# Kernel optimization log

Measured on AMD Instinct MI355X. Metric: run time of the kernel, lower is better.

Reference implementation:

```python
import jax, jax.numpy as jnp
import numpy as np

N_NODES = 50000
N_EDGES = 1_600_000
D_IN, D_HID, D_OUT = 128, 512, 64


def _graph_conv(h, src, dst, W_rel, b_rel, W_root, n_nodes):
    # PyG GraphConv with aggr='add':
    #   out_i = W_rel @ (sum_{j->i} h_j) + b_rel + W_root @ h_i
    agg = jax.ops.segment_sum(h[src], dst, num_segments=n_nodes)  # [N, d]
    return agg @ W_rel + b_rel + h @ W_root


def setup_inputs() -> dict:
    key = jax.random.key(0)
    ks = jax.random.split(key, 12)
    def glorot(k, shape):
        fan_in, fan_out = shape
        lim = (6.0 / (fan_in + fan_out)) ** 0.5
        return jax.random.uniform(k, shape, jnp.float32, -lim, lim)
    x = jax.random.normal(ks[0], (N_NODES, D_IN), jnp.float32)
    edge_index = jax.random.randint(ks[1], (2, N_EDGES), 0, N_NODES, jnp.int64)
    return {
        "x": x,
        "W1_rel": glorot(ks[2], (D_IN, D_HID)),
        "b1": jnp.zeros((D_HID,), jnp.float32),
        "W1_root": glorot(ks[3], (D_IN, D_HID)),
        "W2_rel": glorot(ks[4], (D_HID, D_HID)),
        "b2": jnp.zeros((D_HID,), jnp.float32),
        "W2_root": glorot(ks[5], (D_HID, D_HID)),
        "W3_rel": glorot(ks[6], (D_HID, D_HID)),
        "b3": jnp.zeros((D_HID,), jnp.float32),
        "W3_root": glorot(ks[7], (D_HID, D_HID)),
        "W_lin": glorot(ks[8], (D_HID, D_OUT)),
        "b_lin": jnp.zeros((D_OUT,), jnp.float32),
        "edge_index": edge_index,
    }


def reference(x, W1_rel, b1, W1_root, W2_rel, b2, W2_root,
              W3_rel, b3, W3_root, W_lin, b_lin, edge_index):
    n = x.shape[0]
    src, dst = edge_index[0], edge_index[1]
    h = jax.nn.relu(_graph_conv(x, src, dst, W1_rel, b1, W1_root, n))
    h = jax.nn.relu(_graph_conv(h, src, dst, W2_rel, b2, W2_root, n))
    h = jax.nn.relu(_graph_conv(h, src, dst, W3_rel, b3, W3_root, n))
    node_embed = h
    # dropout is identity in eval mode; final linear head
    logits = h @ W_lin + b_lin
    return (logits, node_embed)
```

## Files before the change

kernel.cpp:

```cpp
#include <hip/hip_runtime.h>


typedef unsigned short u16;
typedef unsigned int u32;
typedef unsigned char u8;

#define NN 50000
#define NE 1600000
#define MPAD 50176
#define GRID_M ((NN + 127) / 128)
#define NBKT 98
#define CAP 20480
#define STG 18432

using frag8 = __attribute__((ext_vector_type(8))) short;
using f32x4 = __attribute__((ext_vector_type(4))) float;
using f32x2 = __attribute__((ext_vector_type(2))) float;

__device__ __forceinline__ u16 f2bf(float f) {
  u32 u = __float_as_uint(f);
  u32 r = u + 0x7fffu + ((u >> 16) & 1u);
  return (u16)(r >> 16);
}
__device__ __forceinline__ float lo2f(u32 u) { return __uint_as_float(u << 16); }
__device__ __forceinline__ float hi2f(u32 u) { return __uint_as_float(u & 0xffff0000u); }
__device__ __forceinline__ u32 pack2(float a, float b) {
  return (u32)f2bf(a) | ((u32)f2bf(b) << 16);
}

__device__ __forceinline__ void g2l16(const void* g, void* l) {
  __builtin_amdgcn_global_load_lds((const __attribute__((address_space(1))) void*)g,
                                   (__attribute__((address_space(3))) void*)l, 16, 0, 0);
}


__global__ void zero_i32(int* p, int n) {
  int i = blockIdx.x * 256 + threadIdx.x;
  if (i < n) p[i] = 0;
}

__global__ __launch_bounds__(256) void p1bin(const int* __restrict__ src,
                                             const int* __restrict__ dst,
                                             int* __restrict__ gcur,
                                             u32* __restrict__ region, int ne) {
  __shared__ u32 lbuf[NBKT * 64];
  __shared__ int lcnt[NBKT];
  __shared__ int gbase[NBKT];
  const int tid = threadIdx.x;
  if (tid < NBKT) lcnt[tid] = 0;
  __syncthreads();
  const int base = blockIdx.x * 2048;
#pragma unroll
  for (int j = 0; j < 8; ++j) {
    int i = base + j * 256 + tid;
    if (i < ne) {
      int d = dst[i];
      int s = src[i];
      int b = d >> 9;
      u32 entry = ((u32)(d & 511) << 16) | (u32)s;
      int slot = atomicAdd(&lcnt[b], 1);
      if (slot < 64) lbuf[b * 64 + slot] = entry;
      else {
        int g = atomicAdd(&gcur[b], 1);
        region[(size_t)b * CAP + g] = entry;
      }
    }
  }
  __syncthreads();
  if (tid < NBKT) {
    int c = min(lcnt[tid], 64);
    gbase[tid] = atomicAdd(&gcur[tid], c);
  }
  __syncthreads();
  const int wv = tid >> 6, lane = tid & 63;
  for (int b = wv; b < NBKT; b += 4) {
    int c = min(lcnt[b], 64);
    int gb = gbase[b];
    for (int s2 = lane; s2 < c; s2 += 64)
      region[(size_t)b * CAP + gb + s2] = lbuf[b * 64 + s2];
  }
}

__global__ void scan98(const int* __restrict__ gcur, int* __restrict__ bbase,
                       int* __restrict__ rs) {
  if (threadIdx.x == 0) {
    int run = 0;
    for (int b = 0; b < NBKT; ++b) {
      bbase[b] = run;
      run += gcur[b];
    }
    bbase[NBKT] = run;
    rs[NN] = run;
  }
}

__global__ __launch_bounds__(256) void p2build(const u32* __restrict__ region,
                                               const int* __restrict__ gcnt,
                                               const int* __restrict__ bbase,
                                               int* __restrict__ rs,
                                               u16* __restrict__ csr) {
  __shared__ int cnt[512];
  __shared__ int off[512];
  __shared__ int sh[256];
  __shared__ u16 stg[STG];
  const int b = blockIdx.x, tid = threadIdx.x;
  const int n0 = b * 512;
  const int nnb = min(512, NN - n0);
  const int ec = gcnt[b];
  const int gb = bbase[b];
  const u32* __restrict__ reg = region + (size_t)b * CAP;
  cnt[tid] = 0;
  cnt[tid + 256] = 0;
  __syncthreads();
  for (int i = tid; i < ec; i += 256) atomicAdd(&cnt[reg[i] >> 16], 1);
  __syncthreads();
  int c0 = cnt[2 * tid], c1 = cnt[2 * tid + 1];
  int s = c0 + c1;
  sh[tid] = s;
  __syncthreads();
  for (int o = 1; o < 256; o <<= 1) {
    int t2 = (tid >= o) ? sh[tid - o] : 0;
    __syncthreads();
    sh[tid] += t2;
    __syncthreads();
  }
  int base0 = sh[tid] - s;
  off[2 * tid] = base0;
  off[2 * tid + 1] = base0 + c0;
  __syncthreads();
  if (2 * tid < nnb) rs[n0 + 2 * tid] = gb + off[2 * tid];
  if (2 * tid + 1 < nnb) rs[n0 + 2 * tid + 1] = gb + off[2 * tid + 1];
  cnt[2 * tid] = off[2 * tid];
  cnt[2 * tid + 1] = off[2 * tid + 1];
  __syncthreads();
  for (int i = tid; i < ec; i += 256) {
    u32 e = reg[i];
    int slot = atomicAdd(&cnt[e >> 16], 1);
    u16 sv = (u16)(e & 0xffff);
    if (slot < STG) stg[slot] = sv;
    else csr[gb + slot] = sv;
  }
  __syncthreads();
  for (int i = tid; i < ec && i < STG; i += 256) csr[gb + i] = stg[i];
}


__global__ void f2bf_x(const float4* __restrict__ in, u16* __restrict__ out, int n4) {
  int i = blockIdx.x * 256 + threadIdx.x;
  if (i < n4) {
    float4 v = in[i];
    int node = i >> 5;
    int w = i & 31;
    uint2 o;
    o.x = pack2(v.x, v.y);
    o.y = pack2(v.z, v.w);
    *(uint2*)(out + (size_t)node * 256 + 128 + w * 4) = o;
  }
}

__global__ void wtrans(const float* __restrict__ Wa, int Ka, const float* __restrict__ Wb,
                       int Kb, int N, u16* __restrict__ out) {
  int idx = blockIdx.x * 256 + threadIdx.x;
  int Kt = Ka + Kb;
  if (idx >= N * Kt) return;
  int n = idx / Kt;
  int k = idx - n * Kt;
  float v = (k < Ka) ? Wa[(size_t)k * N + n] : Wb[(size_t)(k - Ka) * N + n];
  out[idx] = f2bf(v);
}


__global__ __launch_bounds__(256) void agg_bf128(const u16* __restrict__ H, int ldh,
                                                 u16* __restrict__ Out, int ldo,
                                                 const int* __restrict__ rs,
                                                 const u16* __restrict__ csr, int n) {
  int w = (blockIdx.x * 256 + threadIdx.x) >> 6;
  int lane = threadIdx.x & 63;
  if (w >= n) return;
  int beg = rs[w], end = rs[w + 1];
  float a0 = 0.f, a1 = 0.f;
  const size_t lo = (size_t)lane * 2;
  int e = beg;
  for (; e + 4 <= end; e += 4) {
    int s0 = csr[e], s1 = csr[e + 1], s2 = csr[e + 2], s3 = csr[e + 3];
    u32 v0 = *(const u32*)(H + (size_t)s0 * ldh + lo);
    u32 v1 = *(const u32*)(H + (size_t)s1 * ldh + lo);
    u32 v2 = *(const u32*)(H + (size_t)s2 * ldh + lo);
    u32 v3 = *(const u32*)(H + (size_t)s3 * ldh + lo);
    a0 += lo2f(v0); a1 += hi2f(v0);
    a0 += lo2f(v1); a1 += hi2f(v1);
    a0 += lo2f(v2); a1 += hi2f(v2);
    a0 += lo2f(v3); a1 += hi2f(v3);
  }
  for (; e < end; ++e) {
    u32 v = *(const u32*)(H + (size_t)csr[e] * ldh + lo);
    a0 += lo2f(v); a1 += hi2f(v);
  }
  *(u32*)(Out + (size_t)w * ldo + lo) = pack2(a0, a1);
}


__device__ __forceinline__ void accf8(float* a, uint2 v, float s) {
  f32x2 f01 = __builtin_amdgcn_cvt_pk_f32_fp8(v.x, false);
  f32x2 f23 = __builtin_amdgcn_cvt_pk_f32_fp8(v.x, true);
  f32x2 f45 = __builtin_amdgcn_cvt_pk_f32_fp8(v.y, false);
  f32x2 f67 = __builtin_amdgcn_cvt_pk_f32_fp8(v.y, true);
  a[0] = fmaf(f01.x, s, a[0]); a[1] = fmaf(f01.y, s, a[1]);
  a[2] = fmaf(f23.x, s, a[2]); a[3] = fmaf(f23.y, s, a[3]);
  a[4] = fmaf(f45.x, s, a[4]); a[5] = fmaf(f45.y, s, a[5]);
  a[6] = fmaf(f67.x, s, a[6]); a[7] = fmaf(f67.y, s, a[7]);
}

__global__ __launch_bounds__(256) void agg_fp8(const u8* __restrict__ H8,
                                               const float* __restrict__ sc,
                                               u16* __restrict__ Out,
                                               const int* __restrict__ rs,
                                               const u16* __restrict__ csr, int n) {
  int w = (blockIdx.x * 256 + threadIdx.x) >> 6;
  int lane = threadIdx.x & 63;
  if (w >= n) return;
  int beg = rs[w], end = rs[w + 1];
  float acc[8];
#pragma unroll
  for (int i = 0; i < 8; ++i) acc[i] = 0.f;
  const int half = lane >> 5;
  const size_t lo = (size_t)lane * 8;
  int e = beg;
  for (; e + 4 <= end; e += 4) {
    int s0 = csr[e], s1 = csr[e + 1], s2 = csr[e + 2], s3 = csr[e + 3];
    uint2 v0 = *(const uint2*)(H8 + (size_t)s0 * 512 + lo);
    uint2 v1 = *(const uint2*)(H8 + (size_t)s1 * 512 + lo);
    uint2 v2 = *(const uint2*)(H8 + (size_t)s2 * 512 + lo);
    uint2 v3 = *(const uint2*)(H8 + (size_t)s3 * 512 + lo);
    float c0 = sc[s0 * 2 + half];
    float c1 = sc[s1 * 2 + half];
    float c2 = sc[s2 * 2 + half];
    float c3 = sc[s3 * 2 + half];
    accf8(acc, v0, c0); accf8(acc, v1, c1);
    accf8(acc, v2, c2); accf8(acc, v3, c3);
  }
  for (; e < end; ++e) {
    int s0 = csr[e];
    uint2 v = *(const uint2*)(H8 + (size_t)s0 * 512 + lo);
    accf8(acc, v, sc[s0 * 2 + half]);
  }
  uint4 o;
  o.x = pack2(acc[0], acc[1]); o.y = pack2(acc[2], acc[3]);
  o.z = pack2(acc[4], acc[5]); o.w = pack2(acc[6], acc[7]);
  *(uint4*)(Out + (size_t)w * 512 + lo) = o;
}


__global__ __launch_bounds__(512, 4) void gemm256(
    const u16* __restrict__ A1, int lda1, const u16* __restrict__ A2, int lda2, int K1,
    int Ktot, const u16* __restrict__ Bt, const float* __restrict__ bias, int relu,
    u16* __restrict__ out_bf, int ldob, float* __restrict__ out_f32, int ldof,
    u8* __restrict__ out_fp8, float* __restrict__ out_sc, int M) {
  __shared__ u16 lA[128 * 32];
  __shared__ u16 lB[256 * 32];
  __shared__ u32 smaxu[128];
  const int tid = threadIdx.x;
  const int lane = tid & 63;
  const int wv = tid >> 6;
  const int wm = (wv >> 2) * 64;
  const int wn = (wv & 3) * 64;
  const int n0 = blockIdx.x * 256;
  const int m0 = blockIdx.y * 128;
  const int r15 = lane & 15;
  const int quad = lane >> 4;

  if (tid < 128) smaxu[tid] = 0;

  f32x4 acc[4][4];
#pragma unroll
  for (int i = 0; i < 4; ++i)
#pragma unroll
    for (int j = 0; j < 4; ++j) acc[i][j] = (f32x4){0.f, 0.f, 0.f, 0.f};

  for (int kk = 0; kk < Ktot; kk += 32) {
    const u16* Ab;
    int lda;
    if (kk < K1) { Ab = A1 + kk; lda = lda1; }
    else         { Ab = A2 + (kk - K1); lda = lda2; }
    {
      int row = tid >> 2;
      int kc = (tid & 3) * 8;
      g2l16(Ab + (size_t)(m0 + row) * lda + kc, &lA[tid * 8]);
    }
#pragma unroll
    for (int i = 0; i < 2; ++i) {
      int li = tid + i * 512;
      int nrow = li >> 2;
      int kc = (li & 3) * 8;
      g2l16(Bt + (size_t)(n0 + nrow) * Ktot + (kk + kc), &lB[li * 8]);
    }
    __syncthreads();
    frag8 af[4], bfr[4];
#pragma unroll
    for (int mt = 0; mt < 4; ++mt)
      af[mt] = *(const frag8*)&lA[(wm + mt * 16 + r15) * 32 + quad * 8];
#pragma unroll
    for (int nt = 0; nt < 4; ++nt)
      bfr[nt] = *(const frag8*)&lB[(wn + nt * 16 + r15) * 32 + quad * 8];
#pragma unroll
    for (int mt = 0; mt < 4; ++mt)
#pragma unroll
      for (int nt = 0; nt < 4; ++nt)
        acc[mt][nt] =
            __builtin_amdgcn_mfma_f32_16x16x32_bf16(af[mt], bfr[nt], acc[mt][nt], 0, 0, 0);
    __syncthreads();
  }

#pragma unroll
  for (int mt = 0; mt < 4; ++mt) {
#pragma unroll
    for (int r = 0; r < 4; ++r) {
      float rm = 0.f;
#pragma unroll
      for (int nt = 0; nt < 4; ++nt) {
        int c = n0 + wn + nt * 16 + r15;
        float v = acc[mt][nt][r] + bias[c];
        if (relu) v = fmaxf(v, 0.f);
        acc[mt][nt][r] = v;
        rm = fmaxf(rm, v);
      }
      if (out_fp8) {
        rm = fmaxf(rm, __shfl_xor(rm, 1));
        rm = fmaxf(rm, __shfl_xor(rm, 2));
        rm = fmaxf(rm, __shfl_xor(rm, 4));
        rm = fmaxf(rm, __shfl_xor(rm, 8));
        if (r15 == 0) atomicMax(&smaxu[wm + mt * 16 + quad * 4 + r], __float_as_uint(rm));
      }
    }
  }
  if (out_fp8) __syncthreads();

#pragma unroll
  for (int mt = 0; mt < 4; ++mt) {
    int rloc = wm + mt * 16 + quad * 4;
#pragma unroll
    for (int r = 0; r < 4; ++r) {
      int row = m0 + rloc + r;
      if (row < M) {
        float inv = 0.f;
        if (out_fp8) {
          float s = __uint_as_float(smaxu[rloc + r]);
          inv = (s > 0.f) ? 448.f / s : 0.f;
          if (r15 == 0 && wn == 0)
            out_sc[row * 2 + (n0 >> 8)] = (s > 0.f) ? s / 448.f : 0.f;
        }
#pragma unroll
        for (int nt = 0; nt < 4; ++nt) {
          int c = n0 + wn + nt * 16 + r15;
          float v = acc[mt][nt][r];
          if (out_f32) out_f32[(size_t)row * ldof + c] = v;
          if (out_bf) out_bf[(size_t)row * ldob + c] = f2bf(v);
        }
        if (out_fp8) {
          u32 u01 = (u32)__builtin_amdgcn_cvt_pk_fp8_f32(acc[mt][0][r] * inv,
                                                         acc[mt][1][r] * inv, 0, false);
          u32 u23 = (u32)__builtin_amdgcn_cvt_pk_fp8_f32(acc[mt][2][r] * inv,
                                                         acc[mt][3][r] * inv, 0, false);
          size_t rb = (size_t)row * 512 + n0 + wn + r15;
          out_fp8[rb] = (u8)(u01 & 0xff);
          out_fp8[rb + 16] = (u8)((u01 >> 8) & 0xff);
          out_fp8[rb + 32] = (u8)(u23 & 0xff);
          out_fp8[rb + 48] = (u8)((u23 >> 8) & 0xff);
        }
      }
    }
  }
}


__global__ __launch_bounds__(256) void gemm64(
    const u16* __restrict__ A1, int lda1, int Ktot, const u16* __restrict__ Bt,
    const float* __restrict__ bias, float* __restrict__ out_f32, int ldof, int M) {
  __shared__ u16 lA[128 * 32];
  __shared__ u16 lB[64 * 32];
  const int tid = threadIdx.x;
  const int lane = tid & 63;
  const int wv = tid >> 6;
  const int wm = (wv >> 1) * 64;
  const int wn = (wv & 1) * 32;
  const int m0 = blockIdx.x * 128;
  const int r15 = lane & 15;
  const int quad = lane >> 4;

  f32x4 acc[4][2];
#pragma unroll
  for (int i = 0; i < 4; ++i)
#pragma unroll
    for (int j = 0; j < 2; ++j) acc[i][j] = (f32x4){0.f, 0.f, 0.f, 0.f};

  for (int kk = 0; kk < Ktot; kk += 32) {
#pragma unroll
    for (int i = 0; i < 2; ++i) {
      int li = tid + i * 256;
      int row = li >> 2;
      int kc = (li & 3) * 8;
      g2l16(A1 + (size_t)(m0 + row) * lda1 + kk + kc, &lA[li * 8]);
    }
    {
      int nrow = tid >> 2;
      int kc = (tid & 3) * 8;
      if (tid < 256) g2l16(Bt + (size_t)nrow * Ktot + (kk + kc), &lB[tid * 8]);
    }
    __syncthreads();
    frag8 af[4], bfr[2];
#pragma unroll
    for (int mt = 0; mt < 4; ++mt)
      af[mt] = *(const frag8*)&lA[(wm + mt * 16 + r15) * 32 + quad * 8];
#pragma unroll
    for (int nt = 0; nt < 2; ++nt)
      bfr[nt] = *(const frag8*)&lB[(wn + nt * 16 + r15) * 32 + quad * 8];
#pragma unroll
    for (int mt = 0; mt < 4; ++mt)
#pragma unroll
      for (int nt = 0; nt < 2; ++nt)
        acc[mt][nt] =
            __builtin_amdgcn_mfma_f32_16x16x32_bf16(af[mt], bfr[nt], acc[mt][nt], 0, 0, 0);
    __syncthreads();
  }

#pragma unroll
  for (int mt = 0; mt < 4; ++mt) {
    int rbase = m0 + wm + mt * 16 + quad * 4;
#pragma unroll
    for (int r = 0; r < 4; ++r) {
      int row = rbase + r;
      if (row < M) {
#pragma unroll
        for (int nt = 0; nt < 2; ++nt) {
          int c = wn + nt * 16 + r15;
          out_f32[(size_t)row * ldof + c] = acc[mt][nt][r] + bias[c];
        }
      }
    }
  }
}


extern "C" void kernel_launch(void* const* d_in, const int* in_sizes, int n_in, void* d_out,
                              int out_size, void* d_ws, size_t ws_size, hipStream_t stream) {
  const float* x = (const float*)d_in[0];
  const float* W1r = (const float*)d_in[1];
  const float* b1 = (const float*)d_in[2];
  const float* W1o = (const float*)d_in[3];
  const float* W2r = (const float*)d_in[4];
  const float* b2 = (const float*)d_in[5];
  const float* W2o = (const float*)d_in[6];
  const float* W3r = (const float*)d_in[7];
  const float* b3 = (const float*)d_in[8];
  const float* W3o = (const float*)d_in[9];
  const float* Wl = (const float*)d_in[10];
  const float* bl = (const float*)d_in[11];
  const int* src = (const int*)d_in[12];
  const int* dst = src + NE;

  size_t off = 0;
  char* ws = (char*)d_ws;
  auto take = [&](size_t bytes) -> void* {
    void* p = ws + off;
    off = (off + bytes + 255) & ~(size_t)255;
    return p;
  };
  u16* h13 = (u16*)take((size_t)MPAD * 512 * 2);
  u16* h2 = (u16*)take((size_t)MPAD * 512 * 2);
  u16* aggB = (u16*)take((size_t)MPAD * 512 * 2);
  u16* aggx = aggB;
  u8* hfp8 = (u8*)take((size_t)MPAD * 512);
  float* scb = (float*)take((size_t)MPAD * 2 * 4);
  u16* wt1 = (u16*)take((size_t)512 * 256 * 2);
  u16* wt2 = (u16*)take((size_t)512 * 1024 * 2);
  u16* wt3 = (u16*)take((size_t)512 * 1024 * 2);
  u16* wtl = (u16*)take((size_t)64 * 512 * 2);
  u32* region = (u32*)take((size_t)NBKT * CAP * 4);
  int* gcur = (int*)take(128 * 4);
  int* bbase = (int*)take(128 * 4);
  int* rs = (int*)take((size_t)(NN + 1) * 4);
  u16* csr = (u16*)take((size_t)NE * 2);

  float* out_logits = (float*)d_out;
  float* out_embed = out_logits + (size_t)NN * 64;

  zero_i32<<<1, 128, 0, stream>>>(gcur, NBKT);
  p1bin<<<(NE + 2047) / 2048, 256, 0, stream>>>(src, dst, gcur, region, NE);
  scan98<<<1, 64, 0, stream>>>(gcur, bbase, rs);
  p2build<<<NBKT, 256, 0, stream>>>(region, gcur, bbase, rs, csr);

  f2bf_x<<<(NN * 32 + 255) / 256, 256, 0, stream>>>((const float4*)x, aggx, NN * 32);
  wtrans<<<(512 * 256 + 255) / 256, 256, 0, stream>>>(W1r, 128, W1o, 128, 512, wt1);
  wtrans<<<(512 * 1024 + 255) / 256, 256, 0, stream>>>(W2r, 512, W2o, 512, 512, wt2);
  wtrans<<<(512 * 1024 + 255) / 256, 256, 0, stream>>>(W3r, 512, W3o, 512, 512, wt3);
  wtrans<<<(64 * 512 + 255) / 256, 256, 0, stream>>>(Wl, 512, Wl, 0, 64, wtl);

  agg_bf128<<<(NN + 3) / 4, 256, 0, stream>>>(aggx + 128, 256, aggx, 256, rs, csr, NN);
  gemm256<<<dim3(2, GRID_M), 512, 0, stream>>>(aggx, 256, aggx, 256, 256, 256, wt1, b1, 1,
                                               h13, 512, (float*)nullptr, 0, hfp8, scb, NN);
  agg_fp8<<<(NN + 3) / 4, 256, 0, stream>>>(hfp8, scb, aggB, rs, csr, NN);
  gemm256<<<dim3(2, GRID_M), 512, 0, stream>>>(aggB, 512, h13, 512, 512, 1024, wt2, b2, 1,
                                               h2, 512, (float*)nullptr, 0, hfp8, scb, NN);
  agg_fp8<<<(NN + 3) / 4, 256, 0, stream>>>(hfp8, scb, aggB, rs, csr, NN);
  gemm256<<<dim3(2, GRID_M), 512, 0, stream>>>(aggB, 512, h2, 512, 512, 1024, wt3, b3, 1,
                                               h13, 512, out_embed, 512, (u8*)nullptr,
                                               (float*)nullptr, NN);
  gemm64<<<GRID_M, 256, 0, stream>>>(h13, 512, 512, wtl, bl, out_logits, 64, NN);
}
```

Measured before the change: 756.4 us.

## Widen aggregation gathers to 16-byte loads with edge-parallel lanes and shuffle reduction

```diff
diff --git a/kernel.cpp b/kernel.cpp
--- a/kernel.cpp
+++ b/kernel.cpp
@@ -170,6 +170,15 @@
 }
 
 
+__device__ __forceinline__ void accb(f32x2* a, uint4 v, float s) {
+  f32x2 sv = (f32x2){s, s};
+  f32x2 f;
+  f.x = lo2f(v.x); f.y = hi2f(v.x); a[0] += f * sv;
+  f.x = lo2f(v.y); f.y = hi2f(v.y); a[1] += f * sv;
+  f.x = lo2f(v.z); f.y = hi2f(v.z); a[2] += f * sv;
+  f.x = lo2f(v.w); f.y = hi2f(v.w); a[3] += f * sv;
+}
+
 __global__ __launch_bounds__(256) void agg_bf128(const u16* __restrict__ H, int ldh,
                                                  u16* __restrict__ Out, int ldo,
                                                  const int* __restrict__ rs,
@@ -178,37 +187,62 @@
   int lane = threadIdx.x & 63;
   if (w >= n) return;
   int beg = rs[w], end = rs[w + 1];
-  float a0 = 0.f, a1 = 0.f;
-  const size_t lo = (size_t)lane * 2;
+  const int q = lane >> 4;
+  const int lsub = lane & 15;
+  f32x2 acc[4];
+#pragma unroll
+  for (int i = 0; i < 4; ++i) acc[i] = (f32x2){0.f, 0.f};
+
   int e = beg;
-  for (; e + 4 <= end; e += 4) {
-    int s0 = csr[e], s1 = csr[e + 1], s2 = csr[e + 2], s3 = csr[e + 3];
-    u32 v0 = *(const u32*)(H + (size_t)s0 * ldh + lo);
-    u32 v1 = *(const u32*)(H + (size_t)s1 * ldh + lo);
-    u32 v2 = *(const u32*)(H + (size_t)s2 * ldh + lo);
-    u32 v3 = *(const u32*)(H + (size_t)s3 * ldh + lo);
-    a0 += lo2f(v0); a1 += hi2f(v0);
-    a0 += lo2f(v1); a1 += hi2f(v1);
-    a0 += lo2f(v2); a1 += hi2f(v2);
-    a0 += lo2f(v3); a1 += hi2f(v3);
-  }
-  for (; e < end; ++e) {
-    u32 v = *(const u32*)(H + (size_t)csr[e] * ldh + lo);
-    a0 += lo2f(v); a1 += hi2f(v);
-  }
-  *(u32*)(Out + (size_t)w * ldo + lo) = pack2(a0, a1);
-}
-
-
-__device__ __forceinline__ void accf8(float* a, uint2 v, float s) {
-  f32x2 f01 = __builtin_amdgcn_cvt_pk_f32_fp8(v.x, false);
-  f32x2 f23 = __builtin_amdgcn_cvt_pk_f32_fp8(v.x, true);
-  f32x2 f45 = __builtin_amdgcn_cvt_pk_f32_fp8(v.y, false);
-  f32x2 f67 = __builtin_amdgcn_cvt_pk_f32_fp8(v.y, true);
-  a[0] = fmaf(f01.x, s, a[0]); a[1] = fmaf(f01.y, s, a[1]);
-  a[2] = fmaf(f23.x, s, a[2]); a[3] = fmaf(f23.y, s, a[3]);
-  a[4] = fmaf(f45.x, s, a[4]); a[5] = fmaf(f45.y, s, a[5]);
-  a[6] = fmaf(f67.x, s, a[6]); a[7] = fmaf(f67.y, s, a[7]);
+  for (; e + 16 <= end; e += 16) {
+    int si[4];
+#pragma unroll
+    for (int u = 0; u < 4; ++u) si[u] = csr[e + 4 * u + q];
+    uint4 v[4];
+#pragma unroll
+    for (int u = 0; u < 4; ++u)
+      v[u] = *(const uint4*)(H + (size_t)si[u] * ldh + lsub * 8);
+#pragma unroll
+    for (int u = 0; u < 4; ++u) accb(acc, v[u], 1.f);
+  }
+  if (e < end) {
+#pragma unroll
+    for (int u = 0; u < 4; ++u) {
+      int ei = e + 4 * u + q;
+      int ec = min(ei, end - 1);
+      int s0 = csr[ec];
+      uint4 v = *(const uint4*)(H + (size_t)s0 * ldh + lsub * 8);
+      accb(acc, v, (ei < end) ? 1.f : 0.f);
+    }
+  }
+#pragma unroll
+  for (int i = 0; i < 4; ++i) {
+    acc[i].x += __shfl_xor(acc[i].x, 16);
+    acc[i].y += __shfl_xor(acc[i].y, 16);
+    acc[i].x += __shfl_xor(acc[i].x, 32);
+    acc[i].y += __shfl_xor(acc[i].y, 32);
+  }
+  if (lane < 32) {
+    int qq = lane >> 4;
+    uint2 o;
+    o.x = pack2(acc[qq * 2].x, acc[qq * 2].y);
+    o.y = pack2(acc[qq * 2 + 1].x, acc[qq * 2 + 1].y);
+    *(uint2*)(Out + (size_t)w * ldo + (lane & 15) * 8 + qq * 4) = o;
+  }
+}
+
+
+__device__ __forceinline__ void accp(f32x2* a, uint4 v, float s) {
+  f32x2 sv = (f32x2){s, s};
+  f32x2 f;
+  f = __builtin_amdgcn_cvt_pk_f32_fp8(v.x, false); a[0] += f * sv;
+  f = __builtin_amdgcn_cvt_pk_f32_fp8(v.x, true);  a[1] += f * sv;
+  f = __builtin_amdgcn_cvt_pk_f32_fp8(v.y, false); a[2] += f * sv;
+  f = __builtin_amdgcn_cvt_pk_f32_fp8(v.y, true);  a[3] += f * sv;
+  f = __builtin_amdgcn_cvt_pk_f32_fp8(v.z, false); a[4] += f * sv;
+  f = __builtin_amdgcn_cvt_pk_f32_fp8(v.z, true);  a[5] += f * sv;
+  f = __builtin_amdgcn_cvt_pk_f32_fp8(v.w, false); a[6] += f * sv;
+  f = __builtin_amdgcn_cvt_pk_f32_fp8(v.w, true);  a[7] += f * sv;
 }
 
 __global__ __launch_bounds__(256) void agg_fp8(const u8* __restrict__ H8,
@@ -220,34 +254,57 @@
   int lane = threadIdx.x & 63;
   if (w >= n) return;
   int beg = rs[w], end = rs[w + 1];
-  float acc[8];
-#pragma unroll
-  for (int i = 0; i < 8; ++i) acc[i] = 0.f;
-  const int half = lane >> 5;
-  const size_t lo = (size_t)lane * 8;
+  const int halfe = lane >> 5;
+  const int lsub = lane & 31;
+  const int shalf = lsub >> 4;
+  f32x2 acc[8];
+#pragma unroll
+  for (int i = 0; i < 8; ++i) acc[i] = (f32x2){0.f, 0.f};
+
   int e = beg;
-  for (; e + 4 <= end; e += 4) {
-    int s0 = csr[e], s1 = csr[e + 1], s2 = csr[e + 2], s3 = csr[e + 3];
-    uint2 v0 = *(const uint2*)(H8 + (size_t)s0 * 512 + lo);
-    uint2 v1 = *(const uint2*)(H8 + (size_t)s1 * 512 + lo);
-    uint2 v2 = *(const uint2*)(H8 + (size_t)s2 * 512 + lo);
-    uint2 v3 = *(const uint2*)(H8 + (size_t)s3 * 512 + lo);
-    float c0 = sc[s0 * 2 + half];
-    float c1 = sc[s1 * 2 + half];
-    float c2 = sc[s2 * 2 + half];
-    float c3 = sc[s3 * 2 + half];
-    accf8(acc, v0, c0); accf8(acc, v1, c1);
-    accf8(acc, v2, c2); accf8(acc, v3, c3);
-  }
-  for (; e < end; ++e) {
-    int s0 = csr[e];
-    uint2 v = *(const uint2*)(H8 + (size_t)s0 * 512 + lo);
-    accf8(acc, v, sc[s0 * 2 + half]);
+  for (; e + 8 <= end; e += 8) {
+    int si[4];
+#pragma unroll
+    for (int u = 0; u < 4; ++u) si[u] = csr[e + 2 * u + halfe];
+    uint4 v[4];
+#pragma unroll
+    for (int u = 0; u < 4; ++u)
+      v[u] = *(const uint4*)(H8 + (size_t)si[u] * 512 + lsub * 16);
+    float cs[4];
+#pragma unroll
+    for (int u = 0; u < 4; ++u) cs[u] = sc[si[u] * 2 + shalf];
+#pragma unroll
+    for (int u = 0; u < 4; ++u) accp(acc, v[u], cs[u]);
+  }
+  if (e < end) {
+#pragma unroll
+    for (int u = 0; u < 4; ++u) {
+      int ei = e + 2 * u + halfe;
+      int ec = min(ei, end - 1);
+      int s0 = csr[ec];
+      uint4 v = *(const uint4*)(H8 + (size_t)s0 * 512 + lsub * 16);
+      float c = (ei < end) ? sc[s0 * 2 + shalf] : 0.f;
+      accp(acc, v, c);
+    }
+  }
+#pragma unroll
+  for (int i = 0; i < 8; ++i) {
+    acc[i].x += __shfl_xor(acc[i].x, 32);
+    acc[i].y += __shfl_xor(acc[i].y, 32);
   }
   uint4 o;
-  o.x = pack2(acc[0], acc[1]); o.y = pack2(acc[2], acc[3]);
-  o.z = pack2(acc[4], acc[5]); o.w = pack2(acc[6], acc[7]);
-  *(uint4*)(Out + (size_t)w * 512 + lo) = o;
+  if (halfe == 0) {
+    o.x = pack2(acc[0].x, acc[0].y);
+    o.y = pack2(acc[1].x, acc[1].y);
+    o.z = pack2(acc[2].x, acc[2].y);
+    o.w = pack2(acc[3].x, acc[3].y);
+  } else {
+    o.x = pack2(acc[4].x, acc[4].y);
+    o.y = pack2(acc[5].x, acc[5].y);
+    o.z = pack2(acc[6].x, acc[6].y);
+    o.w = pack2(acc[7].x, acc[7].y);
+  }
+  *(uint4*)(Out + (size_t)w * 512 + lsub * 16 + halfe * 8) = o;
 }
 
 
```

Result: no change. 746.3 us (-1.3%).
